# Performance work log

Hardware: AMD Instinct MI355X
Metric: run time of the kernel (lower is better)

## Reference

```python
import jax, jax.numpy as jnp
import numpy as np

D_MODEL = 1024
N_HEADS = 16
D_K = D_MODEL // N_HEADS


def setup_inputs() -> dict:
    key = jax.random.key(0)
    ks = jax.random.split(key, 11)
    B, S = 2, 2048
    scale = 1.0 / np.sqrt(D_MODEL)
    inp = {
        "q": jax.random.normal(ks[0], (B, S, D_MODEL), jnp.float32),
        "k": jax.random.normal(ks[1], (B, S, D_MODEL), jnp.float32),
        "v": jax.random.normal(ks[2], (B, S, D_MODEL), jnp.float32),
        "W_q": jax.random.normal(ks[3], (D_MODEL, D_MODEL), jnp.float32) * scale,
        "b_q": jnp.zeros((D_MODEL,), jnp.float32),
        "W_k": jax.random.normal(ks[4], (D_MODEL, D_MODEL), jnp.float32) * scale,
        "b_k": jnp.zeros((D_MODEL,), jnp.float32),
        "W_v": jax.random.normal(ks[5], (D_MODEL, D_MODEL), jnp.float32) * scale,
        "b_v": jnp.zeros((D_MODEL,), jnp.float32),
        "W_o": jax.random.normal(ks[6], (D_MODEL, D_MODEL), jnp.float32) * scale,
        "b_o": jnp.zeros((D_MODEL,), jnp.float32),
    }
    return inp


def _split_heads(x):
    B, S, _ = x.shape
    return x.reshape(B, S, N_HEADS, D_K).transpose(0, 2, 1, 3)  # [B,H,S,dk]


def reference(q, k, v, W_q, b_q, W_k, b_k, W_v, b_v, W_o, b_o):
    Q = _split_heads(q @ W_q + b_q)
    K = _split_heads(k @ W_k + b_k)
    V = _split_heads(v @ W_v + b_v)
    scores = jnp.einsum("bhqd,bhkd->bhqk", Q, K) / jnp.sqrt(jnp.float32(D_K))
    attn = jax.nn.softmax(scores, axis=-1)  # [B,H,S,S]
    out = jnp.einsum("bhqk,bhkd->bhqd", attn, V)
    B, H, S, dk = out.shape
    out = out.transpose(0, 2, 1, 3).reshape(B, S, H * dk)
    return out @ W_o + b_o, attn
```

## Files before the change

### kernel.cpp

```cpp
#include <hip/hip_runtime.h>
#include <hip/hip_bf16.h>

typedef __bf16 bf16x8 __attribute__((ext_vector_type(8)));
typedef float f32x4 __attribute__((ext_vector_type(4)));
typedef short short4v __attribute__((ext_vector_type(4)));
typedef unsigned short ushort8v __attribute__((ext_vector_type(8)));

#define DEV static __device__ __forceinline__

#if __has_builtin(__builtin_amdgcn_exp2f)
#define EXP2(x) __builtin_amdgcn_exp2f(x)
#else
#define EXP2(x) exp2f(x)
#endif

DEV unsigned short f2bf(float x) {
  union { __hip_bfloat16 b; unsigned short u; } c;
  c.b = __float2bfloat16(x);
  return c.u;
}

DEV unsigned short f2bf_fast(float x) {
  union { float f; unsigned u; } c;
  c.f = x;
  unsigned u = c.u + 0x7fff + ((c.u >> 16) & 1);
  return (unsigned short)(u >> 16);
}

DEV void gload_lds16(const void* g, void* l) {
  __builtin_amdgcn_global_load_lds((const __attribute__((address_space(1))) void*)g,
                                   (__attribute__((address_space(3))) void*)l, 16, 0, 0);
}

__global__ __launch_bounds__(256) void cvt_qkv(const float* __restrict__ q,
                                               const float* __restrict__ k,
                                               const float* __restrict__ v,
                                               unsigned short* __restrict__ qb,
                                               unsigned short* __restrict__ kb,
                                               unsigned short* __restrict__ vb) {
  const float* src = blockIdx.y == 0 ? q : (blockIdx.y == 1 ? k : v);
  unsigned short* dst = blockIdx.y == 0 ? qb : (blockIdx.y == 1 ? kb : vb);
  int idx = (blockIdx.x * 256 + threadIdx.x) * 4;
  float4 xv = *(const float4*)(src + idx);
  ushort4 o;
  o.x = f2bf(xv.x); o.y = f2bf(xv.y); o.z = f2bf(xv.z); o.w = f2bf(xv.w);
  *(ushort4*)(dst + idx) = o;
}

__global__ __launch_bounds__(256) void transpose_all(const float* __restrict__ W0,
                                                     const float* __restrict__ W1,
                                                     const float* __restrict__ W2,
                                                     const float* __restrict__ W3,
                                                     unsigned short* __restrict__ T0,
                                                     unsigned short* __restrict__ T1,
                                                     unsigned short* __restrict__ T2,
                                                     unsigned short* __restrict__ T3) {
  __shared__ float t[64][68];
  int sel = blockIdx.x >> 8;
  const float* W = sel == 0 ? W0 : sel == 1 ? W1 : sel == 2 ? W2 : W3;
  unsigned short* Wt = sel == 0 ? T0 : sel == 1 ? T1 : sel == 2 ? T2 : T3;
  int tile = blockIdx.x & 255;
  int tr = tile >> 4, tc = tile & 15;
  int lr = threadIdx.x >> 4, lc4 = threadIdx.x & 15;
#pragma unroll
  for (int i = 0; i < 4; ++i) {
    int r = i * 16 + lr;
    float4 v = *(const float4*)(W + (size_t)(tr * 64 + r) * 1024 + tc * 64 + lc4 * 4);
    t[r][lc4 * 4 + 0] = v.x; t[r][lc4 * 4 + 1] = v.y;
    t[r][lc4 * 4 + 2] = v.z; t[r][lc4 * 4 + 3] = v.w;
  }
  __syncthreads();
#pragma unroll
  for (int i = 0; i < 4; ++i) {
    int r = i * 16 + lr;
    ushort4 o;
    o.x = f2bf(t[lc4 * 4 + 0][r]);
    o.y = f2bf(t[lc4 * 4 + 1][r]);
    o.z = f2bf(t[lc4 * 4 + 2][r]);
    o.w = f2bf(t[lc4 * 4 + 3][r]);
    *(ushort4*)(Wt + (size_t)(tc * 64 + r) * 1024 + tr * 64 + lc4 * 4) = o;
  }
}

DEV void gemm_core(const unsigned short* __restrict__ A, const unsigned short* __restrict__ Bt,
                   const float* __restrict__ bias, void* __restrict__ Cout,
                   float scale, int mode, int blk,
                   unsigned short* As, unsigned short* Bs) {
  const int tid = threadIdx.x;
  const int l = tid & 63, w = tid >> 6;
  const int wm = w >> 1, wn = w & 1;
  const int r15 = l & 15, kg = l >> 4;
  const int mt = blk >> 3, nt = blk & 7;

  const f32x4 fz = {0.f, 0.f, 0.f, 0.f};
  f32x4 acc[4][4];
#pragma unroll
  for (int i = 0; i < 4; ++i)
#pragma unroll
    for (int j = 0; j < 4; ++j) acc[i][j] = fz;

  for (int kt = 0; kt < 16; ++kt) {
#pragma unroll
    for (int c = 0; c < 4; ++c) {
      int chunk = c * 256 + tid;
      int row = chunk >> 3, slot = chunk & 7;
      int gsl = slot ^ (row & 7);
      gload_lds16(A + (size_t)(mt * 128 + row) * 1024 + kt * 64 + gsl * 8, As + chunk * 8);
      gload_lds16(Bt + (size_t)(nt * 128 + row) * 1024 + kt * 64 + gsl * 8, Bs + chunk * 8);
    }
    __syncthreads();
#pragma unroll
    for (int ks = 0; ks < 2; ++ks) {
      bf16x8 a[4], b[4];
      int slot = ks * 4 + kg;
#pragma unroll
      for (int i = 0; i < 4; ++i) {
        int ra = wm * 64 + i * 16 + r15;
        a[i] = *(const bf16x8*)(As + ra * 64 + (slot ^ (ra & 7)) * 8);
        int rb = wn * 64 + i * 16 + r15;
        b[i] = *(const bf16x8*)(Bs + rb * 64 + (slot ^ (rb & 7)) * 8);
      }
#pragma unroll
      for (int i = 0; i < 4; ++i)
#pragma unroll
        for (int j = 0; j < 4; ++j)
          acc[i][j] = __builtin_amdgcn_mfma_f32_16x16x32_bf16(a[i], b[j], acc[i][j], 0, 0, 0);
    }
    __syncthreads();
  }

#pragma unroll
  for (int j = 0; j < 4; ++j) {
    int gc = nt * 128 + wn * 64 + j * 16 + r15;
    float bj = bias[gc];
#pragma unroll
    for (int i = 0; i < 4; ++i) {
#pragma unroll
      for (int r = 0; r < 4; ++r) {
        int gr = mt * 128 + wm * 64 + i * 16 + kg * 4 + r;
        float val = (acc[i][j][r] + bj) * scale;
        if (mode == 2) {
          ((float*)Cout)[(size_t)gr * 1024 + gc] = val;
        } else {
          int bb = gr >> 11, s = gr & 2047, hh = gc >> 6, dk = gc & 63;
          if (mode == 0)
            ((unsigned short*)Cout)[((size_t)(bb * 16 + hh) * 2048 + s) * 64 + dk] = f2bf(val);
          else
            ((unsigned short*)Cout)[((size_t)(bb * 16 + hh) * 64 + dk) * 2048 + s] = f2bf(val);
        }
      }
    }
  }
}

__global__ __launch_bounds__(256) void gemm_qkv(const unsigned short* __restrict__ qb,
                                                const unsigned short* __restrict__ kb,
                                                const unsigned short* __restrict__ vb,
                                                const unsigned short* __restrict__ Wtq,
                                                const unsigned short* __restrict__ Wtk,
                                                const unsigned short* __restrict__ Wtv,
                                                const float* __restrict__ bq,
                                                const float* __restrict__ bk,
                                                const float* __restrict__ bv,
                                                unsigned short* __restrict__ Qh,
                                                unsigned short* __restrict__ Kh,
                                                unsigned short* __restrict__ Vt) {
  __shared__ unsigned short As[128 * 64];
  __shared__ unsigned short Bs[128 * 64];
  int sel = blockIdx.x >> 8, blk = blockIdx.x & 255;
  const unsigned short* A = sel == 0 ? qb : sel == 1 ? kb : vb;
  const unsigned short* Bt = sel == 0 ? Wtq : sel == 1 ? Wtk : Wtv;
  const float* bias = sel == 0 ? bq : sel == 1 ? bk : bv;
  void* C = sel == 0 ? (void*)Qh : sel == 1 ? (void*)Kh : (void*)Vt;
  gemm_core(A, Bt, bias, C, sel == 0 ? 0.125f * 1.44269504088896f : 1.0f,
            sel == 2 ? 1 : 0, blk, As, Bs);
}

__global__ __launch_bounds__(256) void gemm_out(const unsigned short* __restrict__ AO,
                                                const unsigned short* __restrict__ Wto,
                                                const float* __restrict__ bo,
                                                float* __restrict__ out0) {
  __shared__ unsigned short As[128 * 64];
  __shared__ unsigned short Bs[128 * 64];
  gemm_core(AO, Wto, bo, out0, 1.0f, 2, blockIdx.x, As, Bs);
}

__global__ __launch_bounds__(256) void attn_flash(const unsigned short* __restrict__ Qh,
                                                  const unsigned short* __restrict__ Kh,
                                                  const unsigned short* __restrict__ Vt,
                                                  unsigned short* __restrict__ AO,
                                                  float* __restrict__ rrowG) {
  __shared__ float Ored[4][32][68];
  __shared__ float Ss[4][32];
  __shared__ float rrow[32];

  const int tid = threadIdx.x;
  const int l = tid & 63, w = tid >> 6;
  const int r15 = l & 15, kg = l >> 4;

  const int lb = ((int)blockIdx.x & 7) * 256 + ((int)blockIdx.x >> 3);
  const int bh = lb >> 6;
  const int q0 = (lb & 63) * 32;
  const int b = bh >> 4, h = bh & 15;

  const unsigned short* Kbase = Kh + (size_t)bh * 2048 * 64;
  const unsigned short* Vbase = Vt + (size_t)bh * 64 * 2048;

  bf16x8 aq[2][2];
#pragma unroll
  for (int j = 0; j < 2; ++j)
#pragma unroll
    for (int h2 = 0; h2 < 2; ++h2)
      aq[j][h2] = *(const bf16x8*)(Qh + ((size_t)bh * 2048 + q0 + j * 16 + r15) * 64 +
                                   (h2 * 4 + kg) * 8);

  const f32x4 z4 = {0.f, 0.f, 0.f, 0.f};
  float s2[2] = {0.f, 0.f};
  f32x4 oacc[2][4];
#pragma unroll
  for (int j = 0; j < 2; ++j)
#pragma unroll
    for (int d = 0; d < 4; ++d) oacc[j][d] = z4;

  const int kb0 = w * 16;
  for (int kt = 0; kt < 32; ++kt) {
    const unsigned short* kp = Kbase + (size_t)(kt * 64 + kb0 + r15) * 64;
    bf16x8 kf0 = *(const bf16x8*)(kp + kg * 8);
    bf16x8 kf1 = *(const bf16x8*)(kp + 32 + kg * 8);
    short4v vf[4];
#pragma unroll
    for (int d = 0; d < 4; ++d)
      vf[d] = *(const short4v*)(Vbase + (size_t)(d * 16 + r15) * 2048 + kt * 64 + kb0 + kg * 4);
#pragma unroll
    for (int j = 0; j < 2; ++j) {
      f32x4 sc = __builtin_amdgcn_mfma_f32_16x16x32_bf16(kf0, aq[j][0], z4, 0, 0, 0);
      sc = __builtin_amdgcn_mfma_f32_16x16x32_bf16(kf1, aq[j][1], sc, 0, 0, 0);
      float e0 = EXP2(sc[0]), e1 = EXP2(sc[1]), e2 = EXP2(sc[2]), e3 = EXP2(sc[3]);
      s2[j] += (e0 + e1) + (e2 + e3);
      short4v pf;
      pf[0] = (short)f2bf_fast(e0); pf[1] = (short)f2bf_fast(e1);
      pf[2] = (short)f2bf_fast(e2); pf[3] = (short)f2bf_fast(e3);
#pragma unroll
      for (int d = 0; d < 4; ++d)
        oacc[j][d] = __builtin_amdgcn_mfma_f32_16x16x16bf16_1k(vf[d], pf, oacc[j][d], 0, 0, 0);
    }
  }

#pragma unroll
  for (int j = 0; j < 2; ++j) {
    s2[j] += __shfl_xor(s2[j], 16, 64);
    s2[j] += __shfl_xor(s2[j], 32, 64);
    if (kg == 0) Ss[w][j * 16 + r15] = s2[j];
  }
  __syncthreads();
  if (tid < 32) {
    float s = Ss[0][tid] + Ss[1][tid] + Ss[2][tid] + Ss[3][tid];
    float rv = 1.0f / s;
    rrow[tid] = rv;
    rrowG[(size_t)bh * 2048 + q0 + tid] = rv;
  }
  __syncthreads();

#pragma unroll
  for (int j = 0; j < 2; ++j)
#pragma unroll
    for (int d = 0; d < 4; ++d)
      *(f32x4*)&Ored[w][j * 16 + r15][d * 16 + kg * 4] = oacc[j][d];
  __syncthreads();
  {
    int q = tid >> 3, dc = (tid & 7) * 8;
    float rv = rrow[q];
    ushort8v o;
#pragma unroll
    for (int i = 0; i < 8; ++i) {
      float s = Ored[0][q][dc + i] + Ored[1][q][dc + i] + Ored[2][q][dc + i] + Ored[3][q][dc + i];
      o[i] = f2bf(s * rv);
    }
    *(ushort8v*)(AO + ((size_t)(b * 2048 + q0 + q)) * 1024 + h * 64 + dc) = o;
  }
}

__global__ __launch_bounds__(256) void attn_write(const unsigned short* __restrict__ Qh,
                                                  const unsigned short* __restrict__ Kh,
                                                  const float* __restrict__ rrowG,
                                                  float* __restrict__ attnO) {
  __shared__ float S[4][16][72];

  const int tid = threadIdx.x;
  const int l = tid & 63, w = tid >> 6;
  const int r15 = l & 15, kg = l >> 4;

  const int lb = ((int)blockIdx.x & 7) * 128 + ((int)blockIdx.x >> 3);
  const int bh = lb >> 5;
  const int q0 = (lb & 31) * 64 + w * 16;

  const unsigned short* Kbase = Kh + (size_t)bh * 2048 * 64;
  const unsigned short* Qp = Qh + ((size_t)bh * 2048 + q0 + r15) * 64;
  bf16x8 aq0 = *(const bf16x8*)(Qp + kg * 8);
  bf16x8 aq1 = *(const bf16x8*)(Qp + 32 + kg * 8);

  const float lrv = __log2f(rrowG[(size_t)bh * 2048 + q0 + r15]);

  float* Sw = &S[w][0][0];
  float* attnBase = attnO + ((size_t)bh * 2048 + q0) * 2048;
  const f32x4 z4 = {0.f, 0.f, 0.f, 0.f};

  bf16x8 ka[4][2], kb[4][2];

#define LOADK(KF, c)                                                              \
  {                                                                               \
    const unsigned short* kp_ = Kbase + (size_t)((c) * 64 + r15) * 64 + kg * 8;   \
    _Pragma("unroll")                                                             \
    for (int sub = 0; sub < 4; ++sub) {                                           \
      KF[sub][0] = *(const bf16x8*)(kp_ + sub * 16 * 64);                         \
      KF[sub][1] = *(const bf16x8*)(kp_ + sub * 16 * 64 + 32);                    \
    }                                                                             \
  }

#define PROCESS(KF, c)                                                            \
  {                                                                               \
    _Pragma("unroll")                                                             \
    for (int sub = 0; sub < 4; ++sub) {                                           \
      f32x4 sc = __builtin_amdgcn_mfma_f32_16x16x32_bf16(KF[sub][0], aq0, z4, 0, 0, 0); \
      sc = __builtin_amdgcn_mfma_f32_16x16x32_bf16(KF[sub][1], aq1, sc, 0, 0, 0); \
      f32x4 st = {EXP2(sc[0] + lrv), EXP2(sc[1] + lrv),                           \
                  EXP2(sc[2] + lrv), EXP2(sc[3] + lrv)};                          \
      int col = (sub * 16 + kg * 4) ^ ((r15 & 3) << 4);                           \
      *(f32x4*)(Sw + r15 * 72 + col) = st;                                        \
    }                                                                             \
    _Pragma("unroll")                                                             \
    for (int s = 0; s < 4; ++s) {                                                 \
      int qr = 4 * s + (l >> 4);                                                  \
      int ci = 4 * (l & 15);                                                      \
      int scol = ci ^ ((qr & 3) << 4);                                            \
      f32x4 v = *(const f32x4*)(Sw + qr * 72 + scol);                             \
      *(f32x4*)(attnBase + (size_t)qr * 2048 + (c) * 64 + ci) = v;                \
    }                                                                             \
  }

  LOADK(ka, 0)
  for (int c = 0; c < 32; c += 2) {
    LOADK(kb, c + 1)
    PROCESS(ka, c)
    if (c + 2 < 32) LOADK(ka, c + 2)
    PROCESS(kb, c + 1)
  }
#undef LOADK
#undef PROCESS
}

extern "C" void kernel_launch(void* const* d_in, const int* in_sizes, int n_in,
                              void* d_out, int out_size, void* d_ws, size_t ws_size,
                              hipStream_t stream) {
  const float* q  = (const float*)d_in[0];
  const float* k  = (const float*)d_in[1];
  const float* v  = (const float*)d_in[2];
  const float* Wq = (const float*)d_in[3];
  const float* bq = (const float*)d_in[4];
  const float* Wk = (const float*)d_in[5];
  const float* bk = (const float*)d_in[6];
  const float* Wv = (const float*)d_in[7];
  const float* bvp = (const float*)d_in[8];
  const float* Wo = (const float*)d_in[9];
  const float* bo = (const float*)d_in[10];

  char* wsb = (char*)d_ws;
  const size_t MB = (size_t)1 << 20;
  unsigned short* qb  = (unsigned short*)(wsb + 0 * MB);
  unsigned short* kbp = (unsigned short*)(wsb + 8 * MB);
  unsigned short* vbp = (unsigned short*)(wsb + 16 * MB);
  unsigned short* Wtq = (unsigned short*)(wsb + 24 * MB);
  unsigned short* Wtk = (unsigned short*)(wsb + 26 * MB);
  unsigned short* Wtv = (unsigned short*)(wsb + 28 * MB);
  unsigned short* Wto = (unsigned short*)(wsb + 30 * MB);
  unsigned short* Qh  = (unsigned short*)(wsb + 32 * MB);
  unsigned short* Kh  = (unsigned short*)(wsb + 40 * MB);
  unsigned short* Vt  = (unsigned short*)(wsb + 48 * MB);
  unsigned short* AO  = (unsigned short*)(wsb + 56 * MB);
  float* rrowG = (float*)(wsb + 0 * MB);

  float* attnO = (float*)d_out + (size_t)2 * 2048 * 1024;

  cvt_qkv<<<dim3(4096, 3), 256, 0, stream>>>(q, k, v, qb, kbp, vbp);
  transpose_all<<<1024, 256, 0, stream>>>(Wq, Wk, Wv, Wo, Wtq, Wtk, Wtv, Wto);
  gemm_qkv<<<768, 256, 0, stream>>>(qb, kbp, vbp, Wtq, Wtk, Wtv, bq, bk, bvp, Qh, Kh, Vt);
  attn_flash<<<2048, 256, 0, stream>>>(Qh, Kh, Vt, AO, rrowG);
  attn_write<<<1024, 256, 0, stream>>>(Qh, Kh, rrowG, attnO);
  gemm_out<<<256, 256, 0, stream>>>(AO, Wto, bo, (float*)d_out);
}
```

Measured before the change: 450.4 us.

## Restructure attn_write to stage full bf16 probability rows in LDS and stream them out

```diff
diff --git a/kernel.cpp b/kernel.cpp
--- a/kernel.cpp
+++ b/kernel.cpp
@@ -20,12 +20,12 @@
   return c.u;
 }
 
-DEV unsigned short f2bf_fast(float x) {
+DEV unsigned f2bf_fast_u(float x) {
   union { float f; unsigned u; } c;
   c.f = x;
-  unsigned u = c.u + 0x7fff + ((c.u >> 16) & 1);
-  return (unsigned short)(u >> 16);
-}
+  return (c.u + 0x7fff + ((c.u >> 16) & 1)) >> 16;
+}
+DEV unsigned short f2bf_fast(float x) { return (unsigned short)f2bf_fast_u(x); }
 
 DEV void gload_lds16(const void* g, void* l) {
   __builtin_amdgcn_global_load_lds((const __attribute__((address_space(1))) void*)g,
@@ -284,15 +284,15 @@
                                                   const unsigned short* __restrict__ Kh,
                                                   const float* __restrict__ rrowG,
                                                   float* __restrict__ attnO) {
-  __shared__ float S[4][16][72];
+  __shared__ unsigned short Pl[16 * 2048];
 
   const int tid = threadIdx.x;
   const int l = tid & 63, w = tid >> 6;
   const int r15 = l & 15, kg = l >> 4;
 
-  const int lb = ((int)blockIdx.x & 7) * 128 + ((int)blockIdx.x >> 3);
-  const int bh = lb >> 5;
-  const int q0 = (lb & 31) * 64 + w * 16;
+  const int lb = ((int)blockIdx.x & 7) * 512 + ((int)blockIdx.x >> 3);
+  const int bh = lb >> 7;
+  const int q0 = (lb & 127) * 16;
 
   const unsigned short* Kbase = Kh + (size_t)bh * 2048 * 64;
   const unsigned short* Qp = Qh + ((size_t)bh * 2048 + q0 + r15) * 64;
@@ -301,15 +301,15 @@
 
   const float lrv = __log2f(rrowG[(size_t)bh * 2048 + q0 + r15]);
 
-  float* Sw = &S[w][0][0];
-  float* attnBase = attnO + ((size_t)bh * 2048 + q0) * 2048;
   const f32x4 z4 = {0.f, 0.f, 0.f, 0.f};
+  const int kq = w * 512;
+  char* Plb = (char*)Pl;
 
   bf16x8 ka[4][2], kb[4][2];
 
 #define LOADK(KF, c)                                                              \
   {                                                                               \
-    const unsigned short* kp_ = Kbase + (size_t)((c) * 64 + r15) * 64 + kg * 8;   \
+    const unsigned short* kp_ = Kbase + (size_t)(kq + (c) * 64 + r15) * 64 + kg * 8; \
     _Pragma("unroll")                                                             \
     for (int sub = 0; sub < 4; ++sub) {                                           \
       KF[sub][0] = *(const bf16x8*)(kp_ + sub * 16 * 64);                         \
@@ -323,30 +323,43 @@
     for (int sub = 0; sub < 4; ++sub) {                                           \
       f32x4 sc = __builtin_amdgcn_mfma_f32_16x16x32_bf16(KF[sub][0], aq0, z4, 0, 0, 0); \
       sc = __builtin_amdgcn_mfma_f32_16x16x32_bf16(KF[sub][1], aq1, sc, 0, 0, 0); \
-      f32x4 st = {EXP2(sc[0] + lrv), EXP2(sc[1] + lrv),                           \
-                  EXP2(sc[2] + lrv), EXP2(sc[3] + lrv)};                          \
-      int col = (sub * 16 + kg * 4) ^ ((r15 & 3) << 4);                           \
-      *(f32x4*)(Sw + r15 * 72 + col) = st;                                        \
+      unsigned u0 = f2bf_fast_u(EXP2(sc[0] + lrv)) | (f2bf_fast_u(EXP2(sc[1] + lrv)) << 16); \
+      unsigned u1 = f2bf_fast_u(EXP2(sc[2] + lrv)) | (f2bf_fast_u(EXP2(sc[3] + lrv)) << 16); \
+      int colb = (kq + (c) * 64 + sub * 16 + kg * 4) * 2;                         \
+      uint2 uu = {u0, u1};                                                        \
+      *(uint2*)(Plb + r15 * 4096 + (colb ^ ((r15 & 7) << 4))) = uu;               \
     }                                                                             \
-    _Pragma("unroll")                                                             \
-    for (int s = 0; s < 4; ++s) {                                                 \
-      int qr = 4 * s + (l >> 4);                                                  \
-      int ci = 4 * (l & 15);                                                      \
-      int scol = ci ^ ((qr & 3) << 4);                                            \
-      f32x4 v = *(const f32x4*)(Sw + qr * 72 + scol);                             \
-      *(f32x4*)(attnBase + (size_t)qr * 2048 + (c) * 64 + ci) = v;                \
-    }                                                                             \
   }
 
   LOADK(ka, 0)
-  for (int c = 0; c < 32; c += 2) {
+  for (int c = 0; c < 8; c += 2) {
     LOADK(kb, c + 1)
     PROCESS(ka, c)
-    if (c + 2 < 32) LOADK(ka, c + 2)
+    if (c + 2 < 8) LOADK(ka, c + 2)
     PROCESS(kb, c + 1)
   }
 #undef LOADK
 #undef PROCESS
+
+  __syncthreads();
+
+  float* wavep = attnO + ((size_t)bh * 2048 + q0 + w * 4) * 2048;
+#pragma unroll
+  for (int ri = 0; ri < 4; ++ri) {
+    int qr = w * 4 + ri;
+    const char* rowl = Plb + qr * 4096;
+    int swz = (qr & 7) << 4;
+    float* rowp = wavep + (size_t)ri * 2048 + l * 4;
+#pragma unroll
+    for (int seg = 0; seg < 8; ++seg) {
+      uint2 u = *(const uint2*)(rowl + ((seg * 512 + l * 8) ^ swz));
+      union { unsigned u; float f; } c0, c1, c2, c3;
+      c0.u = u.x << 16; c1.u = u.x & 0xffff0000u;
+      c2.u = u.y << 16; c3.u = u.y & 0xffff0000u;
+      f32x4 v = {c0.f, c1.f, c2.f, c3.f};
+      __builtin_nontemporal_store(v, (f32x4*)(rowp + seg * 256));
+    }
+  }
 }
 
 extern "C" void kernel_launch(void* const* d_in, const int* in_sizes, int n_in,
@@ -385,6 +398,6 @@
   transpose_all<<<1024, 256, 0, stream>>>(Wq, Wk, Wv, Wo, Wtq, Wtk, Wtv, Wto);
   gemm_qkv<<<768, 256, 0, stream>>>(qb, kbp, vbp, Wtq, Wtk, Wtv, bq, bk, bvp, Qh, Kh, Vt);
   attn_flash<<<2048, 256, 0, stream>>>(Qh, Kh, Vt, AO, rrowG);
-  attn_write<<<1024, 256, 0, stream>>>(Qh, Kh, rrowG, attnO);
+  attn_write<<<4096, 256, 0, stream>>>(Qh, Kh, rrowG, attnO);
   gemm_out<<<256, 256, 0, stream>>>(AO, Wto, bo, (float*)d_out);
 }
```

Result: faster. 412.7 us (-8.4%).
